# Kernel tuning notes

Hardware: AMD Instinct MI355X
Metric: run time of the kernel (lower is better)

## Reference

```python
import jax, jax.numpy as jnp
import numpy as np

D_CONV = 4
D_STATE = 16
DT_RANK = 64  # ceil(1024/16)


def _forward(x, W_in, conv_w, conv_b, W_x, W_dt, b_dt, A_log, Dp, W_out):
    B, L, Dm = x.shape
    d_inner = W_dt.shape[0]
    # in_proj: (B,L,Dm) @ (2*d_inner, Dm)^T
    xz = jnp.einsum('bld,ed->ble', x, W_in)
    xc, z = jnp.split(xz, 2, axis=-1)  # each (B,L,d_inner)
    # depthwise causal conv1d (torch pads both sides by d_conv-1 then truncates to L == left-pad only)
    xt = jnp.swapaxes(xc, 1, 2)  # (B, d_inner, L)
    conv = jax.lax.conv_general_dilated(
        xt, conv_w[:, None, :], window_strides=(1,),
        padding=[(D_CONV - 1, 0)], feature_group_count=d_inner)
    xconv = jax.nn.silu(jnp.swapaxes(conv, 1, 2) + conv_b)  # (B,L,d_inner)
    # x_proj -> dt_low, B, C
    x_dbl = jnp.einsum('bld,ed->ble', xconv, W_x)
    dt_low = x_dbl[..., :DT_RANK]
    Bp = x_dbl[..., DT_RANK:DT_RANK + D_STATE]      # (B,L,N)
    Cp = x_dbl[..., DT_RANK + D_STATE:]             # (B,L,N)
    dt = jax.nn.softplus(jnp.einsum('blr,dr->bld', dt_low, W_dt) + b_dt)  # (B,L,d_inner)
    A = -jnp.exp(A_log)  # (d_inner, N)

    # recurrence h_t = exp(dt_t * A) * h_{t-1} + dt_t * B_t * x_t ; y_t = <h_t, C_t>
    def step(h, inp):
        dt_t, B_t, C_t, x_t = inp  # (B,D),(B,N),(B,N),(B,D)
        dA = jnp.exp(dt_t[..., None] * A)                      # (B,D,N)
        dBx = dt_t[..., None] * B_t[:, None, :] * x_t[..., None]
        h = dA * h + dBx
        y = jnp.einsum('bdn,bn->bd', h, C_t)
        return h, y

    h0 = jnp.zeros((B, d_inner, D_STATE), dtype=x.dtype)
    xs = (jnp.swapaxes(dt, 0, 1), jnp.swapaxes(Bp, 0, 1),
          jnp.swapaxes(Cp, 0, 1), jnp.swapaxes(xconv, 0, 1))
    _, ys = jax.lax.scan(step, h0, xs)  # ys: (L,B,d_inner)
    y = jnp.swapaxes(ys, 0, 1) + xconv * Dp  # skip connection with D
    out = jnp.einsum('bld,ed->ble', y * jax.nn.silu(z), W_out)
    return out


def setup_inputs() -> dict:
    key = jax.random.key(0)
    ks = jax.random.split(key, 8)
    B, L, d_model = 2, 1024, 1024
    d_inner = 2 * d_model
    x = jax.random.normal(ks[0], (B, L, d_model), dtype=jnp.float32)
    W_in = jax.random.normal(ks[1], (2 * d_inner, d_model), dtype=jnp.float32) / np.sqrt(d_model)
    conv_w = jax.random.normal(ks[2], (d_inner, D_CONV), dtype=jnp.float32) / np.sqrt(D_CONV)
    conv_b = jnp.zeros((d_inner,), dtype=jnp.float32)
    W_x = jax.random.normal(ks[3], (DT_RANK + 2 * D_STATE, d_inner), dtype=jnp.float32) / np.sqrt(d_inner)
    W_dt = jax.random.uniform(ks[4], (d_inner, DT_RANK), minval=-1.0, maxval=1.0, dtype=jnp.float32) * DT_RANK ** -0.5
    dt = jnp.exp(jax.random.uniform(ks[5], (d_inner,), dtype=jnp.float32)
                 * (np.log(0.1) - np.log(0.001)) + np.log(0.001))
    b_dt = dt + jnp.log(-jnp.expm1(-dt))  # softplus inverse init
    A_log = jnp.log(jnp.tile(jnp.arange(1, D_STATE + 1, dtype=jnp.float32), (d_inner, 1)))
    Dp = jnp.ones((d_inner,), dtype=jnp.float32)
    W_out = jax.random.normal(ks[6], (d_model, d_inner), dtype=jnp.float32) / np.sqrt(d_inner)
    return {'x': x, 'W_in': W_in, 'conv_w': conv_w, 'conv_b': conv_b, 'W_x': W_x,
            'W_dt': W_dt, 'b_dt': b_dt, 'A_log': A_log, 'Dp': Dp, 'W_out': W_out}


def reference(x, W_in, conv_w, conv_b, W_x, W_dt, b_dt, A_log, Dp, W_out):
    return _forward(x, W_in, conv_w, conv_b, W_x, W_dt, b_dt, A_log, Dp, W_out)
```

## Files before the change

kernel.cpp:

```cpp
#include <hip/hip_runtime.h>
#include <hip/hip_bf16.h>
#include <math.h>

constexpr int Bb  = 2;
constexpr int Ls  = 1024;
constexpr int DM  = 1024;
constexpr int DI  = 2048;
constexpr int DXZ = 4096;
constexpr int DXD = 96;
constexpr int DTR = 64;
constexpr int DST = 16;
constexpr int NCH = 8;
constexpr int CHL = 128;
constexpr int ML  = Bb * Ls;

typedef __attribute__((ext_vector_type(8))) short bf16x8;
typedef __attribute__((ext_vector_type(4))) float f32x4;

__device__ __forceinline__ float sigmoidf_(float v) {
    return 1.0f / (1.0f + __expf(-v));
}

__device__ __forceinline__ int pk_bf16(float lo, float hi) {
    unsigned int ul = __float_as_uint(lo);
    ul += 0x7fffu + ((ul >> 16) & 1u);
    unsigned int uh = __float_as_uint(hi);
    uh += 0x7fffu + ((uh >> 16) & 1u);
    return (int)((ul >> 16) | (uh & 0xffff0000u));
}

template <int CTRL>
__device__ __forceinline__ float dpp_add_(float v) {
    int t = __builtin_amdgcn_update_dpp(
        0, __float_as_int(v), CTRL, 0xF, 0xF, true);
    return v + __int_as_float(t);
}
__device__ __forceinline__ float red16_(float p) {
    p = dpp_add_<0xB1>(p);
    p = dpp_add_<0x4E>(p);
    p = dpp_add_<0x141>(p);
    p = dpp_add_<0x140>(p);
    return p;
}

__device__ __forceinline__ int swz(int row, int chunk) {
    return (((row << 2) + chunk) ^ (row & 7)) << 3;
}

template <int SPLIT>
__global__ __launch_bounds__(256) void gemm_bf16_f32in(
    const float* __restrict__ A, int lda,
    const float* __restrict__ W, int ldw,
    float* __restrict__ C, float* __restrict__ C2, int ldc, int K)
{
    __shared__ __align__(16) unsigned short As[128 * 32];
    __shared__ __align__(16) unsigned short Ws[128 * 32];

    const int tid  = threadIdx.x;
    const int lane = tid & 63;
    const int wave = tid >> 6;
    const int bm = blockIdx.y * 128;
    const int bn = blockIdx.x * 128;

    const int srow = tid >> 1;
    const int cb   = (tid & 1) * 2;
    const float* Ag = A + (size_t)(bm + srow) * lda + cb * 8;
    const float* Wg = W + (size_t)(bn + srow) * ldw + cb * 8;
    const int ia0 = swz(srow, cb);
    const int ia1 = swz(srow, cb + 1);

    const int wr = (wave >> 1) * 64;
    const int wc = (wave & 1) * 64;
    const int fr = lane & 15;
    const int fq = lane >> 4;

    f32x4 acc[4][4];
#pragma unroll
    for (int m = 0; m < 4; ++m)
#pragma unroll
        for (int n = 0; n < 4; ++n) acc[m][n] = (f32x4){0.f, 0.f, 0.f, 0.f};

    for (int k0 = 0; k0 < K; k0 += 32) {
        const float4 a0 = *(const float4*)(Ag + k0);
        const float4 a1 = *(const float4*)(Ag + k0 + 4);
        const float4 a2 = *(const float4*)(Ag + k0 + 8);
        const float4 a3 = *(const float4*)(Ag + k0 + 12);
        const float4 w0 = *(const float4*)(Wg + k0);
        const float4 w1 = *(const float4*)(Wg + k0 + 4);
        const float4 w2 = *(const float4*)(Wg + k0 + 8);
        const float4 w3 = *(const float4*)(Wg + k0 + 12);

        __syncthreads();
        {
            const int4 pa0 = {pk_bf16(a0.x, a0.y), pk_bf16(a0.z, a0.w),
                              pk_bf16(a1.x, a1.y), pk_bf16(a1.z, a1.w)};
            const int4 pa1 = {pk_bf16(a2.x, a2.y), pk_bf16(a2.z, a2.w),
                              pk_bf16(a3.x, a3.y), pk_bf16(a3.z, a3.w)};
            const int4 pw0 = {pk_bf16(w0.x, w0.y), pk_bf16(w0.z, w0.w),
                              pk_bf16(w1.x, w1.y), pk_bf16(w1.z, w1.w)};
            const int4 pw1 = {pk_bf16(w2.x, w2.y), pk_bf16(w2.z, w2.w),
                              pk_bf16(w3.x, w3.y), pk_bf16(w3.z, w3.w)};
            *(int4*)(As + ia0) = pa0;
            *(int4*)(As + ia1) = pa1;
            *(int4*)(Ws + ia0) = pw0;
            *(int4*)(Ws + ia1) = pw1;
        }
        __syncthreads();

        bf16x8 af[4], bfv[4];
#pragma unroll
        for (int m = 0; m < 4; ++m)
            af[m] = *(const bf16x8*)(As + swz(wr + m * 16 + fr, fq));
#pragma unroll
        for (int n = 0; n < 4; ++n)
            bfv[n] = *(const bf16x8*)(Ws + swz(wc + n * 16 + fr, fq));
#pragma unroll
        for (int m = 0; m < 4; ++m)
#pragma unroll
            for (int n = 0; n < 4; ++n)
                acc[m][n] = __builtin_amdgcn_mfma_f32_16x16x32_bf16(
                    af[m], bfv[n], acc[m][n], 0, 0, 0);
    }

#pragma unroll
    for (int m = 0; m < 4; ++m)
#pragma unroll
        for (int n = 0; n < 4; ++n) {
            const int col = bn + wc + n * 16 + fr;
#pragma unroll
            for (int j = 0; j < 4; ++j) {
                const int row = bm + wr + m * 16 + fq * 4 + j;
                const float v = acc[m][n][j];
                if (SPLIT) {
                    if (col < DI) {
                        C[(size_t)row * ldc + col] = v;
                    } else {
                        C2[(size_t)row * ldc + (col - DI)] = v * sigmoidf_(v);
                    }
                } else {
                    C[(size_t)row * ldc + col] = v;
                }
            }
        }
}

template <int EPI>
__global__ __launch_bounds__(256) void gemm_nt(
    const float* __restrict__ A, int lda,
    const float* __restrict__ W, int ldw,
    float* __restrict__ C, int ldc,
    int N, int K, const float* __restrict__ bias, int za, int zw, int zc)
{
    A += (size_t)blockIdx.z * za;
    W += (size_t)blockIdx.z * zw;
    C += (size_t)blockIdx.z * zc;

    __shared__ float Asl[16][132];
    __shared__ float Wsl[16][132];

    const int tid = threadIdx.x;
    const int tx = tid & 15;
    const int ty = tid >> 4;
    const int bm = blockIdx.y * 128;
    const int bn = blockIdx.x * 128;

    const int lr = tid >> 1;
    const int lk = (tid & 1) * 8;

    float acc[8][8];
#pragma unroll
    for (int i = 0; i < 8; ++i)
#pragma unroll
        for (int j = 0; j < 8; ++j) acc[i][j] = 0.0f;

    const float* Ap = A + (size_t)(bm + lr) * lda + lk;
    const float* Wp = W + (size_t)(bn + lr) * ldw + lk;
    const bool wok = (bn + lr) < N;
    const float4 f4z = make_float4(0.f, 0.f, 0.f, 0.f);

    for (int k0 = 0; k0 < K; k0 += 16) {
        const float4 av0 = *(const float4*)(Ap + k0);
        const float4 av1 = *(const float4*)(Ap + k0 + 4);
        const float4 wv0 = wok ? *(const float4*)(Wp + k0)     : f4z;
        const float4 wv1 = wok ? *(const float4*)(Wp + k0 + 4) : f4z;

        __syncthreads();
        Asl[lk + 0][lr] = av0.x; Asl[lk + 1][lr] = av0.y;
        Asl[lk + 2][lr] = av0.z; Asl[lk + 3][lr] = av0.w;
        Asl[lk + 4][lr] = av1.x; Asl[lk + 5][lr] = av1.y;
        Asl[lk + 6][lr] = av1.z; Asl[lk + 7][lr] = av1.w;
        Wsl[lk + 0][lr] = wv0.x; Wsl[lk + 1][lr] = wv0.y;
        Wsl[lk + 2][lr] = wv0.z; Wsl[lk + 3][lr] = wv0.w;
        Wsl[lk + 4][lr] = wv1.x; Wsl[lk + 5][lr] = wv1.y;
        Wsl[lk + 6][lr] = wv1.z; Wsl[lk + 7][lr] = wv1.w;
        __syncthreads();

#pragma unroll
        for (int k = 0; k < 16; ++k) {
            const float4 a0 = *(const float4*)&Asl[k][(ty << 2)];
            const float4 a1 = *(const float4*)&Asl[k][64 + (ty << 2)];
            const float4 b0 = *(const float4*)&Wsl[k][(tx << 2)];
            const float4 b1 = *(const float4*)&Wsl[k][64 + (tx << 2)];
            const float ar[8] = {a0.x, a0.y, a0.z, a0.w, a1.x, a1.y, a1.z, a1.w};
            const float br[8] = {b0.x, b0.y, b0.z, b0.w, b1.x, b1.y, b1.z, b1.w};
#pragma unroll
            for (int i = 0; i < 8; ++i)
#pragma unroll
                for (int j = 0; j < 8; ++j)
                    acc[i][j] = fmaf(ar[i], br[j], acc[i][j]);
        }
    }

#pragma unroll
    for (int i = 0; i < 8; ++i) {
        const int row = bm + ((i & 4) << 4) + (ty << 2) + (i & 3);
#pragma unroll
        for (int j = 0; j < 8; ++j) {
            const int col = bn + ((j & 4) << 4) + (tx << 2) + (j & 3);
            if (col < N) {
                float v = acc[i][j];
                if (EPI == 2) {
                    v += bias[row];
                    v = (v > 20.f) ? v : log1pf(__expf(v));
                }
                C[(size_t)row * ldc + col] = v;
            }
        }
    }
}

__global__ __launch_bounds__(256) void reduce_xdbl_kernel(
    const float* __restrict__ part, float* __restrict__ xdbl,
    float* __restrict__ bcT)
{
    const int idx = blockIdx.x * 256 + threadIdx.x;
    if (idx >= ML * DXD) return;
    const int m = idx / DXD;
    const int j = idx - m * DXD;
    const float* p = part + (size_t)m * 768 + j;
    float s = 0.0f;
#pragma unroll
    for (int kc = 0; kc < 8; ++kc) s += p[kc * DXD];
    xdbl[idx] = s;
    if (j >= DTR) bcT[(size_t)(j - DTR) * ML + m] = s;
}

__global__ __launch_bounds__(256) void conv_silu_kernel(
    const float* __restrict__ xc,
    const float* __restrict__ conv_w,
    const float* __restrict__ conv_b,
    float* __restrict__ xconv)
{
    const int idx = blockIdx.x * 256 + threadIdx.x;
    const int d  = idx & (DI - 1);
    const int bl = idx >> 11;
    const int l  = bl & (Ls - 1);

    const float4 cw = *(const float4*)(conv_w + (d << 2));
    const float w[4] = {cw.x, cw.y, cw.z, cw.w};
    float acc = conv_b[d];
    const float* base = xc + (size_t)bl * DI + d;
#pragma unroll
    for (int j = 0; j < 4; ++j) {
        const int ll = l - 3 + j;
        if (ll >= 0) acc += base[(j - 3) * DI] * w[j];
    }
    xconv[idx] = acc * sigmoidf_(acc);
}

__global__ __launch_bounds__(256) void scan_pass1(
    const float* __restrict__ dtT,
    const float* __restrict__ xconv,
    const float* __restrict__ bcT,
    const float* __restrict__ A_log,
    float* __restrict__ hend, float* __restrict__ Dprod)
{
    const int b    = blockIdx.z;
    const int c    = blockIdx.y;
    const int lane = threadIdx.x & 63;
    const int wave = threadIdx.x >> 6;
    const int n    = lane & 15;
    const int dl   = lane >> 4;
    const int d    = blockIdx.x * 16 + wave * 4 + dl;
    const int m0   = b * Ls + c * CHL;

    const float Anat = -__expf(A_log[(d << 4) + n]);

    const float4* dtp = (const float4*)(dtT + (size_t)d * ML + m0);
    const float4* Bp  = (const float4*)(bcT + (size_t)n * ML + m0);
    const float*  xq  = xconv + (size_t)m0 * DI + d;

    float4 dt4 = dtp[0], B4 = Bp[0];
    float h = 0.0f, S = 0.0f;

    for (int it = 0; it < CHL / 4; ++it) {
        const float4 dtc = dt4, Bc = B4;
        if (it + 1 < CHL / 4) { dt4 = dtp[it + 1]; B4 = Bp[it + 1]; }
#pragma unroll
        for (int i = 0; i < 4; ++i) {
            const float dtv = ((const float*)&dtc)[i];
            const float Bn  = ((const float*)&Bc)[i];
            const float xv  = *xq; xq += DI;
            S += dtv;
            const float e = __expf(dtv * Anat);
            h = fmaf(e, h, dtv * xv * Bn);
        }
    }

    const size_t idx = (((size_t)(b * NCH + c) * DI + d) << 4) + n;
    hend[idx]  = h;
    Dprod[idx] = __expf(Anat * S);
}

__global__ __launch_bounds__(256) void scan_pass2(
    const float* __restrict__ dtT,
    float* __restrict__ xconv,
    const float* __restrict__ bcT,
    const float* __restrict__ zg,
    const float* __restrict__ A_log,
    const float* __restrict__ Dp,
    const float* __restrict__ hend, const float* __restrict__ Dprod)
{
    const int b    = blockIdx.z;
    const int c    = blockIdx.y;
    const int lane = threadIdx.x & 63;
    const int wave = threadIdx.x >> 6;
    const int n    = lane & 15;
    const int dl   = lane >> 4;
    const int d    = blockIdx.x * 16 + wave * 4 + dl;
    const int m0   = b * Ls + c * CHL;

    const float Anat = -__expf(A_log[(d << 4) + n]);
    const float dpd  = Dp[d];

    float h = 0.0f;
    for (int cp = 0; cp < c; ++cp) {
        const size_t off = (((size_t)(b * NCH + cp) * DI + d) << 4) + n;
        h = fmaf(Dprod[off], h, hend[off]);
    }

    const float4* dtp = (const float4*)(dtT + (size_t)d * ML + m0);
    const float4* Bp  = (const float4*)(bcT + (size_t)n * ML + m0);
    const float4* Cp  = (const float4*)(bcT + (size_t)(DST + n) * ML + m0);
    float* xq = xconv + (size_t)m0 * DI + d;
    const ptrdiff_t zoff = zg - (const float*)xconv;

    float4 dt4 = dtp[0], B4 = Bp[0], C4 = Cp[0];

    for (int it = 0; it < CHL / 4; ++it) {
        const float4 dtc = dt4, Bc = B4, Cc = C4;
        if (it + 1 < CHL / 4) {
            dt4 = dtp[it + 1]; B4 = Bp[it + 1]; C4 = Cp[it + 1];
        }
#pragma unroll
        for (int i = 0; i < 4; ++i) {
            const float dtv = ((const float*)&dtc)[i];
            const float Bn  = ((const float*)&Bc)[i];
            const float Cn  = ((const float*)&Cc)[i];
            const float xv  = *xq;
            const float e = __expf(dtv * Anat);
            h = fmaf(e, h, dtv * xv * Bn);
            float p = red16_(h * Cn);
            if (n == 0) {
                const float zgv = xq[zoff];
                *xq = fmaf(xv, dpd, p) * zgv;
            }
            xq += DI;
        }
    }
}

extern "C" void kernel_launch(void* const* d_in, const int* in_sizes, int n_in,
                              void* d_out, int out_size, void* d_ws, size_t ws_size,
                              hipStream_t stream)
{
    const float* x      = (const float*)d_in[0];
    const float* W_in   = (const float*)d_in[1];
    const float* conv_w = (const float*)d_in[2];
    const float* conv_b = (const float*)d_in[3];
    const float* W_x    = (const float*)d_in[4];
    const float* W_dt   = (const float*)d_in[5];
    const float* b_dt   = (const float*)d_in[6];
    const float* A_log  = (const float*)d_in[7];
    const float* Dp     = (const float*)d_in[8];
    const float* W_out  = (const float*)d_in[9];
    float* out = (float*)d_out;

    float* ws     = (float*)d_ws;
    float* xc_arr = ws;
    float* zg_arr = xc_arr + (size_t)ML * DI;
    float* xconv  = zg_arr + (size_t)ML * DI;
    float* xdbl   = xconv  + (size_t)ML * DI;

    float* hend  = out;
    float* Dprod = hend + (size_t)Bb * NCH * DI * DST;
    float* bcT   = Dprod + (size_t)Bb * NCH * DI * DST;

    float* dtT   = xc_arr;
    const dim3 blk(256);

    gemm_bf16_f32in<1><<<dim3(DXZ / 128, ML / 128), blk, 0, stream>>>(
        x, DM, W_in, DM, xc_arr, zg_arr, DI, DM);

    conv_silu_kernel<<<dim3((ML * DI) / 256), blk, 0, stream>>>(
        xc_arr, conv_w, conv_b, xconv);

    gemm_nt<0><<<dim3(1, ML / 128, 8), blk, 0, stream>>>(
        xconv, DI, W_x, DI, xc_arr, 768, DXD, DI / 8, nullptr,
        DI / 8, DI / 8, DXD);
    reduce_xdbl_kernel<<<dim3((ML * DXD + 255) / 256), blk, 0, stream>>>(
        xc_arr, xdbl, bcT);

    gemm_nt<2><<<dim3(ML / 128, DI / 128), blk, 0, stream>>>(
        W_dt, DTR, xdbl, DXD, dtT, ML, ML, DTR, b_dt, 0, 0, 0);

    scan_pass1<<<dim3(DI / 16, NCH - 1, Bb), blk, 0, stream>>>(
        dtT, xconv, bcT, A_log, hend, Dprod);
    scan_pass2<<<dim3(DI / 16, NCH, Bb), blk, 0, stream>>>(
        dtT, xconv, bcT, zg_arr, A_log, Dp, hend, Dprod);

    gemm_bf16_f32in<0><<<dim3(DM / 128, ML / 128), blk, 0, stream>>>(
        xconv, DI, W_out, DI, out, nullptr, DM, DI);
}
```

Measured before the change: 503.3 us.

## Store conv output channel-major so scan reads contiguous, gate into bf16 for out-proj

The conv+SiLU kernel now writes its output transposed (d-major, time-contiguous) through an LDS tile. The scan passes can then read x and write y as float4 vectors instead of strided per-timestep loads. The x_proj GEMM gains a transposed-A path to consume that layout. A new gate_transpose kernel multiplies y by the silu(z) gate, transposes back and packs to bf16, and the out-projection GEMM loads bf16 A directly. This adds an extra kernel and transpose pass in exchange for coalesced scan memory traffic and halved A bandwidth in the final GEMM.

```diff
diff --git a/kernel.cpp b/kernel.cpp
--- a/kernel.cpp
+++ b/kernel.cpp
@@ -47,9 +47,9 @@
     return (((row << 2) + chunk) ^ (row & 7)) << 3;
 }
 
-template <int SPLIT>
+template <int SPLIT, int ABF16>
 __global__ __launch_bounds__(256) void gemm_bf16_f32in(
-    const float* __restrict__ A, int lda,
+    const void* __restrict__ Av, int lda,
     const float* __restrict__ W, int ldw,
     float* __restrict__ C, float* __restrict__ C2, int ldc, int K)
 {
@@ -64,7 +64,10 @@
 
     const int srow = tid >> 1;
     const int cb   = (tid & 1) * 2;
-    const float* Ag = A + (size_t)(bm + srow) * lda + cb * 8;
+    const float* Ag = (ABF16 ? nullptr
+                             : (const float*)Av + (size_t)(bm + srow) * lda + cb * 8);
+    const unsigned short* Ag16 = (ABF16
+        ? (const unsigned short*)Av + (size_t)(bm + srow) * lda + cb * 8 : nullptr);
     const float* Wg = W + (size_t)(bn + srow) * ldw + cb * 8;
     const int ia0 = swz(srow, cb);
     const int ia1 = swz(srow, cb + 1);
@@ -81,10 +84,20 @@
         for (int n = 0; n < 4; ++n) acc[m][n] = (f32x4){0.f, 0.f, 0.f, 0.f};
 
     for (int k0 = 0; k0 < K; k0 += 32) {
-        const float4 a0 = *(const float4*)(Ag + k0);
-        const float4 a1 = *(const float4*)(Ag + k0 + 4);
-        const float4 a2 = *(const float4*)(Ag + k0 + 8);
-        const float4 a3 = *(const float4*)(Ag + k0 + 12);
+        int4 pa0, pa1;
+        if (ABF16) {
+            pa0 = *(const int4*)(Ag16 + k0);
+            pa1 = *(const int4*)(Ag16 + k0 + 8);
+        } else {
+            const float4 a0 = *(const float4*)(Ag + k0);
+            const float4 a1 = *(const float4*)(Ag + k0 + 4);
+            const float4 a2 = *(const float4*)(Ag + k0 + 8);
+            const float4 a3 = *(const float4*)(Ag + k0 + 12);
+            pa0 = (int4){pk_bf16(a0.x, a0.y), pk_bf16(a0.z, a0.w),
+                         pk_bf16(a1.x, a1.y), pk_bf16(a1.z, a1.w)};
+            pa1 = (int4){pk_bf16(a2.x, a2.y), pk_bf16(a2.z, a2.w),
+                         pk_bf16(a3.x, a3.y), pk_bf16(a3.z, a3.w)};
+        }
         const float4 w0 = *(const float4*)(Wg + k0);
         const float4 w1 = *(const float4*)(Wg + k0 + 4);
         const float4 w2 = *(const float4*)(Wg + k0 + 8);
@@ -92,10 +105,6 @@
 
         __syncthreads();
         {
-            const int4 pa0 = {pk_bf16(a0.x, a0.y), pk_bf16(a0.z, a0.w),
-                              pk_bf16(a1.x, a1.y), pk_bf16(a1.z, a1.w)};
-            const int4 pa1 = {pk_bf16(a2.x, a2.y), pk_bf16(a2.z, a2.w),
-                              pk_bf16(a3.x, a3.y), pk_bf16(a3.z, a3.w)};
             const int4 pw0 = {pk_bf16(w0.x, w0.y), pk_bf16(w0.z, w0.w),
                               pk_bf16(w1.x, w1.y), pk_bf16(w1.z, w1.w)};
             const int4 pw1 = {pk_bf16(w2.x, w2.y), pk_bf16(w2.z, w2.w),
@@ -144,7 +153,7 @@
         }
 }
 
-template <int EPI>
+template <int EPI, int ATRANS>
 __global__ __launch_bounds__(256) void gemm_nt(
     const float* __restrict__ A, int lda,
     const float* __restrict__ W, int ldw,
@@ -166,6 +175,8 @@
 
     const int lr = tid >> 1;
     const int lk = (tid & 1) * 8;
+    const int krow = tid >> 4;
+    const int mseg = (tid & 15) * 8;
 
     float acc[8][8];
 #pragma unroll
@@ -173,22 +184,35 @@
 #pragma unroll
         for (int j = 0; j < 8; ++j) acc[i][j] = 0.0f;
 
-    const float* Ap = A + (size_t)(bm + lr) * lda + lk;
+    const float* Ap = ATRANS
+        ? A + (size_t)krow * lda + bm + mseg
+        : A + (size_t)(bm + lr) * lda + lk;
     const float* Wp = W + (size_t)(bn + lr) * ldw + lk;
     const bool wok = (bn + lr) < N;
     const float4 f4z = make_float4(0.f, 0.f, 0.f, 0.f);
 
     for (int k0 = 0; k0 < K; k0 += 16) {
-        const float4 av0 = *(const float4*)(Ap + k0);
-        const float4 av1 = *(const float4*)(Ap + k0 + 4);
+        float4 av0, av1;
+        if (ATRANS) {
+            av0 = *(const float4*)(Ap + (size_t)k0 * lda);
+            av1 = *(const float4*)(Ap + (size_t)k0 * lda + 4);
+        } else {
+            av0 = *(const float4*)(Ap + k0);
+            av1 = *(const float4*)(Ap + k0 + 4);
+        }
         const float4 wv0 = wok ? *(const float4*)(Wp + k0)     : f4z;
         const float4 wv1 = wok ? *(const float4*)(Wp + k0 + 4) : f4z;
 
         __syncthreads();
-        Asl[lk + 0][lr] = av0.x; Asl[lk + 1][lr] = av0.y;
-        Asl[lk + 2][lr] = av0.z; Asl[lk + 3][lr] = av0.w;
-        Asl[lk + 4][lr] = av1.x; Asl[lk + 5][lr] = av1.y;
-        Asl[lk + 6][lr] = av1.z; Asl[lk + 7][lr] = av1.w;
+        if (ATRANS) {
+            *(float4*)&Asl[krow][mseg]     = av0;
+            *(float4*)&Asl[krow][mseg + 4] = av1;
+        } else {
+            Asl[lk + 0][lr] = av0.x; Asl[lk + 1][lr] = av0.y;
+            Asl[lk + 2][lr] = av0.z; Asl[lk + 3][lr] = av0.w;
+            Asl[lk + 4][lr] = av1.x; Asl[lk + 5][lr] = av1.y;
+            Asl[lk + 6][lr] = av1.z; Asl[lk + 7][lr] = av1.w;
+        }
         Wsl[lk + 0][lr] = wv0.x; Wsl[lk + 1][lr] = wv0.y;
         Wsl[lk + 2][lr] = wv0.z; Wsl[lk + 3][lr] = wv0.w;
         Wsl[lk + 4][lr] = wv1.x; Wsl[lk + 5][lr] = wv1.y;
@@ -245,32 +269,57 @@
     if (j >= DTR) bcT[(size_t)(j - DTR) * ML + m] = s;
 }
 
-__global__ __launch_bounds__(256) void conv_silu_kernel(
+constexpr int CT_LDS = 260;
+__global__ __launch_bounds__(256) void conv_transpose_kernel(
     const float* __restrict__ xc,
     const float* __restrict__ conv_w,
     const float* __restrict__ conv_b,
-    float* __restrict__ xconv)
-{
-    const int idx = blockIdx.x * 256 + threadIdx.x;
-    const int d  = idx & (DI - 1);
-    const int bl = idx >> 11;
-    const int l  = bl & (Ls - 1);
-
+    float* __restrict__ xT)
+{
+    __shared__ float tile[32][CT_LDS];
+    const int d0 = blockIdx.x * 32;
+    const int m0 = blockIdx.y * 256;
+    const int t  = threadIdx.x;
+    const bool atStart = ((m0 & (Ls - 1)) == 0);
+
+    for (int rg = 0; rg < 33; ++rg) {
+        const int r = rg * 8 + (t >> 5) - 3;
+        const int dcol = t & 31;
+        if (r <= 255) {
+            float v = 0.0f;
+            if (r >= 0 || !atStart)
+                v = xc[(size_t)(m0 + r) * DI + d0 + dcol];
+            tile[dcol][3 + r] = v;
+        }
+    }
+    __syncthreads();
+
+    const int dd  = t >> 3;
+    const int seg = (t & 7) * 32;
+    const int d   = d0 + dd;
     const float4 cw = *(const float4*)(conv_w + (d << 2));
-    const float w[4] = {cw.x, cw.y, cw.z, cw.w};
-    float acc = conv_b[d];
-    const float* base = xc + (size_t)bl * DI + d;
-#pragma unroll
-    for (int j = 0; j < 4; ++j) {
-        const int ll = l - 3 + j;
-        if (ll >= 0) acc += base[(j - 3) * DI] * w[j];
-    }
-    xconv[idx] = acc * sigmoidf_(acc);
+    const float  cb = conv_b[d];
+    float* dst = xT + (size_t)d * ML + m0 + seg;
+
+    float4 cur = *(const float4*)&tile[dd][seg];
+#pragma unroll
+    for (int g = 0; g < 8; ++g) {
+        const float4 nxt = *(const float4*)&tile[dd][seg + 4 * g + 4];
+        const float a0 = cb + cw.x*cur.x + cw.y*cur.y + cw.z*cur.z + cw.w*cur.w;
+        const float a1 = cb + cw.x*cur.y + cw.y*cur.z + cw.z*cur.w + cw.w*nxt.x;
+        const float a2 = cb + cw.x*cur.z + cw.y*cur.w + cw.z*nxt.x + cw.w*nxt.y;
+        const float a3 = cb + cw.x*cur.w + cw.y*nxt.x + cw.z*nxt.y + cw.w*nxt.z;
+        float4 o;
+        o.x = a0 * sigmoidf_(a0); o.y = a1 * sigmoidf_(a1);
+        o.z = a2 * sigmoidf_(a2); o.w = a3 * sigmoidf_(a3);
+        *(float4*)(dst + 4 * g) = o;
+        cur = nxt;
+    }
 }
 
 __global__ __launch_bounds__(256) void scan_pass1(
     const float* __restrict__ dtT,
-    const float* __restrict__ xconv,
+    const float* __restrict__ xT,
     const float* __restrict__ bcT,
     const float* __restrict__ A_log,
     float* __restrict__ hend, float* __restrict__ Dprod)
@@ -287,20 +336,22 @@
     const float Anat = -__expf(A_log[(d << 4) + n]);
 
     const float4* dtp = (const float4*)(dtT + (size_t)d * ML + m0);
+    const float4* xp  = (const float4*)(xT  + (size_t)d * ML + m0);
     const float4* Bp  = (const float4*)(bcT + (size_t)n * ML + m0);
-    const float*  xq  = xconv + (size_t)m0 * DI + d;
-
-    float4 dt4 = dtp[0], B4 = Bp[0];
+
+    float4 dt4 = dtp[0], x4 = xp[0], B4 = Bp[0];
     float h = 0.0f, S = 0.0f;
 
     for (int it = 0; it < CHL / 4; ++it) {
-        const float4 dtc = dt4, Bc = B4;
-        if (it + 1 < CHL / 4) { dt4 = dtp[it + 1]; B4 = Bp[it + 1]; }
+        const float4 dtc = dt4, xc4 = x4, Bc = B4;
+        if (it + 1 < CHL / 4) {
+            dt4 = dtp[it + 1]; x4 = xp[it + 1]; B4 = Bp[it + 1];
+        }
 #pragma unroll
         for (int i = 0; i < 4; ++i) {
             const float dtv = ((const float*)&dtc)[i];
+            const float xv  = ((const float*)&xc4)[i];
             const float Bn  = ((const float*)&Bc)[i];
-            const float xv  = *xq; xq += DI;
             S += dtv;
             const float e = __expf(dtv * Anat);
             h = fmaf(e, h, dtv * xv * Bn);
@@ -314,9 +365,8 @@
 
 __global__ __launch_bounds__(256) void scan_pass2(
     const float* __restrict__ dtT,
-    float* __restrict__ xconv,
+    float* xT,
     const float* __restrict__ bcT,
-    const float* __restrict__ zg,
     const float* __restrict__ A_log,
     const float* __restrict__ Dp,
     const float* __restrict__ hend, const float* __restrict__ Dprod)
@@ -340,33 +390,64 @@
     }
 
     const float4* dtp = (const float4*)(dtT + (size_t)d * ML + m0);
+    const float4* xp  = (const float4*)(xT  + (size_t)d * ML + m0);
     const float4* Bp  = (const float4*)(bcT + (size_t)n * ML + m0);
     const float4* Cp  = (const float4*)(bcT + (size_t)(DST + n) * ML + m0);
-    float* xq = xconv + (size_t)m0 * DI + d;
-    const ptrdiff_t zoff = zg - (const float*)xconv;
-
-    float4 dt4 = dtp[0], B4 = Bp[0], C4 = Cp[0];
+    float4* yq = (float4*)(xT + (size_t)d * ML + m0);
+
+    float4 dt4 = dtp[0], x4 = xp[0], B4 = Bp[0], C4 = Cp[0];
 
     for (int it = 0; it < CHL / 4; ++it) {
-        const float4 dtc = dt4, Bc = B4, Cc = C4;
+        const float4 dtc = dt4, xc4 = x4, Bc = B4, Cc = C4;
         if (it + 1 < CHL / 4) {
-            dt4 = dtp[it + 1]; B4 = Bp[it + 1]; C4 = Cp[it + 1];
-        }
+            dt4 = dtp[it + 1]; x4 = xp[it + 1];
+            B4 = Bp[it + 1];   C4 = Cp[it + 1];
+        }
+        float4 y4;
 #pragma unroll
         for (int i = 0; i < 4; ++i) {
             const float dtv = ((const float*)&dtc)[i];
+            const float xv  = ((const float*)&xc4)[i];
             const float Bn  = ((const float*)&Bc)[i];
             const float Cn  = ((const float*)&Cc)[i];
-            const float xv  = *xq;
             const float e = __expf(dtv * Anat);
             h = fmaf(e, h, dtv * xv * Bn);
-            float p = red16_(h * Cn);
-            if (n == 0) {
-                const float zgv = xq[zoff];
-                *xq = fmaf(xv, dpd, p) * zgv;
-            }
-            xq += DI;
-        }
+            const float p = red16_(h * Cn);
+            ((float*)&y4)[i] = fmaf(xv, dpd, p);
+        }
+        if (n == 0) yq[it] = y4;
+    }
+}
+
+__global__ __launch_bounds__(256) void gate_transpose_kernel(
+    const float* __restrict__ yT,
+    const float* __restrict__ zg,
+    unsigned short* __restrict__ yb)
+{
+    __shared__ float Ty[64][65];
+    __shared__ float Tz[64][65];
+    const int d0 = blockIdx.x * 64;
+    const int m0 = blockIdx.y * 64;
+    const int t  = threadIdx.x;
+    const int cc = t & 63, r4 = t >> 6;
+
+#pragma unroll 4
+    for (int rr = 0; rr < 16; ++rr) {
+        const int r = rr * 4 + r4;
+        Ty[r][cc] = yT[(size_t)(d0 + r) * ML + m0 + cc];
+        Tz[r][cc] = zg[(size_t)(m0 + r) * DI + d0 + cc];
+    }
+    __syncthreads();
+
+    const int dp  = (t & 31) * 2;
+    const int mr4 = t >> 5;
+#pragma unroll 4
+    for (int rr = 0; rr < 8; ++rr) {
+        const int mr = rr * 8 + mr4;
+        const float v0 = Ty[dp][mr]     * Tz[mr][dp];
+        const float v1 = Ty[dp + 1][mr] * Tz[mr][dp + 1];
+        *(unsigned int*)(yb + (size_t)(m0 + mr) * DI + d0 + dp) =
+            (unsigned int)pk_bf16(v0, v1);
     }
 }
 
@@ -389,36 +470,41 @@
     float* ws     = (float*)d_ws;
     float* xc_arr = ws;
     float* zg_arr = xc_arr + (size_t)ML * DI;
-    float* xconv  = zg_arr + (size_t)ML * DI;
-    float* xdbl   = xconv  + (size_t)ML * DI;
+    float* xT_arr = zg_arr + (size_t)ML * DI;
+    float* xdbl   = xT_arr + (size_t)ML * DI;
 
     float* hend  = out;
     float* Dprod = hend + (size_t)Bb * NCH * DI * DST;
     float* bcT   = Dprod + (size_t)Bb * NCH * DI * DST;
 
-    float* dtT   = xc_arr;
+    float* dtT = xc_arr;
+    unsigned short* ybf = (unsigned short*)xc_arr;
+
     const dim3 blk(256);
 
-    gemm_bf16_f32in<1><<<dim3(DXZ / 128, ML / 128), blk, 0, stream>>>(
+    gemm_bf16_f32in<1, 0><<<dim3(DXZ / 128, ML / 128), blk, 0, stream>>>(
         x, DM, W_in, DM, xc_arr, zg_arr, DI, DM);
 
-    conv_silu_kernel<<<dim3((ML * DI) / 256), blk, 0, stream>>>(
-        xc_arr, conv_w, conv_b, xconv);
-
-    gemm_nt<0><<<dim3(1, ML / 128, 8), blk, 0, stream>>>(
-        xconv, DI, W_x, DI, xc_arr, 768, DXD, DI / 8, nullptr,
-        DI / 8, DI / 8, DXD);
+    conv_transpose_kernel<<<dim3(DI / 32, ML / 256), blk, 0, stream>>>(
+        xc_arr, conv_w, conv_b, xT_arr);
+
+    gemm_nt<0, 1><<<dim3(1, ML / 128, 8), blk, 0, stream>>>(
+        xT_arr, ML, W_x, DI, xc_arr, 768, DXD, DI / 8, nullptr,
+        (DI / 8) * ML, DI / 8, DXD);
     reduce_xdbl_kernel<<<dim3((ML * DXD + 255) / 256), blk, 0, stream>>>(
         xc_arr, xdbl, bcT);
 
-    gemm_nt<2><<<dim3(ML / 128, DI / 128), blk, 0, stream>>>(
+    gemm_nt<2, 0><<<dim3(ML / 128, DI / 128), blk, 0, stream>>>(
         W_dt, DTR, xdbl, DXD, dtT, ML, ML, DTR, b_dt, 0, 0, 0);
 
     scan_pass1<<<dim3(DI / 16, NCH - 1, Bb), blk, 0, stream>>>(
-        dtT, xconv, bcT, A_log, hend, Dprod);
+        dtT, xT_arr, bcT, A_log, hend, Dprod);
     scan_pass2<<<dim3(DI / 16, NCH, Bb), blk, 0, stream>>>(
-        dtT, xconv, bcT, zg_arr, A_log, Dp, hend, Dprod);
-
-    gemm_bf16_f32in<0><<<dim3(DM / 128, ML / 128), blk, 0, stream>>>(
-        xconv, DI, W_out, DI, out, nullptr, DM, DI);
-}
+        dtT, xT_arr, bcT, A_log, Dp, hend, Dprod);
+
+    gate_transpose_kernel<<<dim3(DI / 64, ML / 64), blk, 0, stream>>>(
+        xT_arr, zg_arr, ybf);
+
+    gemm_bf16_f32in<0, 1><<<dim3(DM / 128, ML / 128), blk, 0, stream>>>(
+        ybf, DI, W_out, DI, out, nullptr, DM, DI);
+}
```

New measurement: 446.8 us. 11.2% less time.
